# Performance work log

Hardware: AMD Instinct MI355X
Metric: run time of the kernel (lower is better)

The kernel has to match this reference:

```python
import jax, jax.numpy as jnp
import numpy as np

FP8_MAX = 448.0  # max finite value of float8_e4m3fn
EPS = 1e-12


def _quantize_fp8(t):
    """Per-tensor dynamic fp8 quantization: returns (fp8_tensor, scale) where
    dequant = fp8.astype(f32) / scale, matching the torch module's math."""
    t32 = t.astype(jnp.float32)
    amax = jnp.maximum(jnp.max(jnp.abs(t32)), EPS)
    scale = FP8_MAX / amax
    t_fp8 = jnp.clip(t32 * scale, -FP8_MAX, FP8_MAX).astype(jnp.float8_e4m3fn)
    return t_fp8, scale


def setup_inputs() -> dict:
    key = jax.random.key(0)
    kx, kw, kb = jax.random.split(key, 3)
    M, K, N = 4096, 4096, 4096  # tokens, in_features, out_features
    x = jax.random.normal(kx, (M, K), dtype=jnp.float16)
    weight = jax.random.normal(kw, (N, K), dtype=jnp.float16)
    bias = jax.random.normal(kb, (N,), dtype=jnp.float16)
    return {"x": x, "weight": weight, "bias": bias}


def reference(x, weight, bias):
    # weight pre-quantization (quantize_weight)
    w_fp8, w_scale = _quantize_fp8(weight)
    # dynamic activation quantization
    x_fp8, x_scale = _quantize_fp8(x)
    # scaled_mm: (x_fp8 @ w_fp8.T) * scale_a * scale_b, out fp16
    acc = jnp.einsum(
        "mk,nk->mn",
        x_fp8.astype(jnp.float32),
        w_fp8.astype(jnp.float32),
        preferred_element_type=jnp.float32,
    )
    out = (acc * (1.0 / x_scale) * (1.0 / w_scale)).astype(jnp.float16)
    out = out + bias
    return out
```

## Files before the change

kernel.cpp:

```cpp
#include <hip/hip_runtime.h>
#include <hip/hip_fp16.h>

typedef __bf16 bf16x8 __attribute__((ext_vector_type(8)));
typedef float f32x4 __attribute__((ext_vector_type(4)));
typedef int i32x8 __attribute__((ext_vector_type(8)));
typedef unsigned short ushort8 __attribute__((ext_vector_type(8)));

#define BM 256
#define BN 128
#define BK 128
#define FP8MAX 448.0f
#define SCALE_ONE 0x7F7F7F7FU
#define A_BYTES (BM * BK)
#define B_BYTES (BN * BK)
#define SLOT_BYTES (A_BYTES + B_BYTES)

__global__ __launch_bounds__(256)
void amax_stage1(const float* __restrict__ x, unsigned n4x,
                 const float* __restrict__ w, unsigned n4w,
                 float* __restrict__ bm) {
    __shared__ float wmax[4];
    bool isw = blockIdx.x >= 1024;
    const float* in = isw ? w : x;
    unsigned n4 = isw ? n4w : n4x;
    unsigned tid = (blockIdx.x & 1023) * 256 + threadIdx.x;
    float m = 0.f;
    for (unsigned i = tid; i < n4; i += 1024 * 256) {
        float4 v = *(const float4*)(in + (size_t)i * 4);
        m = fmaxf(m, fmaxf(fmaxf(fabsf(v.x), fabsf(v.y)), fmaxf(fabsf(v.z), fabsf(v.w))));
    }
#pragma unroll
    for (int off = 32; off > 0; off >>= 1)
        m = fmaxf(m, __shfl_down(m, off));
    if ((threadIdx.x & 63) == 0) wmax[threadIdx.x >> 6] = m;
    __syncthreads();
    if (threadIdx.x == 0)
        bm[blockIdx.x] = fmaxf(fmaxf(wmax[0], wmax[1]), fmaxf(wmax[2], wmax[3]));
}

__global__ __launch_bounds__(256)
void amax_stage2(const float* __restrict__ bm, float* __restrict__ outv) {
    __shared__ float wmax[4];
    const float* p = bm + (size_t)blockIdx.x * 1024;
    float m = 0.f;
    for (int i = threadIdx.x; i < 1024; i += 256) m = fmaxf(m, p[i]);
#pragma unroll
    for (int off = 32; off > 0; off >>= 1)
        m = fmaxf(m, __shfl_down(m, off));
    if ((threadIdx.x & 63) == 0) wmax[threadIdx.x >> 6] = m;
    __syncthreads();
    if (threadIdx.x == 0)
        outv[blockIdx.x] = fmaxf(fmaxf(wmax[0], wmax[1]), fmaxf(wmax[2], wmax[3]));
}

__global__ __launch_bounds__(256)
void quant_kernel(const float* __restrict__ x, unsigned n8x,
                  const float* __restrict__ w, unsigned n8w,
                  unsigned char* __restrict__ xq, unsigned char* __restrict__ wq,
                  const float* __restrict__ amax2) {
    bool isw = blockIdx.x >= 2048;
    const float* in = isw ? w : x;
    uint2* out = (uint2*)(isw ? wq : xq);
    unsigned n8 = isw ? n8w : n8x;
    float amax = fmaxf(amax2[isw ? 1 : 0], 1e-12f);
    float scale = FP8MAX / amax;
    unsigned tid = (blockIdx.x & 2047) * 256 + threadIdx.x;
    for (unsigned i = tid; i < n8; i += 2048 * 256) {
        float4 lo = *(const float4*)(in + (size_t)i * 8);
        float4 hi = *(const float4*)(in + (size_t)i * 8 + 4);
        float f[8] = {lo.x, lo.y, lo.z, lo.w, hi.x, hi.y, hi.z, hi.w};
#pragma unroll
        for (int j = 0; j < 8; ++j)
            f[j] = fminf(fmaxf(f[j] * scale, -FP8MAX), FP8MAX);
        unsigned w0 = __builtin_amdgcn_cvt_pk_fp8_f32(f[0], f[1], 0u, false);
        w0 = __builtin_amdgcn_cvt_pk_fp8_f32(f[2], f[3], w0, true);
        unsigned w1 = __builtin_amdgcn_cvt_pk_fp8_f32(f[4], f[5], 0u, false);
        w1 = __builtin_amdgcn_cvt_pk_fp8_f32(f[6], f[7], w1, true);
        out[i] = make_uint2(w0, w1);
    }
}

__device__ inline void gl2lds16(const void* g, void* l) {
    __builtin_amdgcn_global_load_lds(
        (const __attribute__((address_space(1))) unsigned int*)g,
        (__attribute__((address_space(3))) unsigned int*)l, 16, 0, 0);
}

__global__ __launch_bounds__(512, 2)
void gemm_kernel(const unsigned char* __restrict__ A,
                 const unsigned char* __restrict__ B,
                 const float* __restrict__ bias,
                 float* __restrict__ C,
                 const float* __restrict__ amax2,
                 int M, int N, int K) {
    extern __shared__ char LDS[];

    int tid = threadIdx.x;
    int lane = tid & 63;
    int wave = tid >> 6;
    int wr = wave >> 1;
    int wc = wave & 1;
    int row0 = blockIdx.y * BM;
    int col0 = blockIdx.x * BN;

    f32x4 acc[4][4];
#pragma unroll
    for (int m = 0; m < 4; ++m)
#pragma unroll
        for (int n = 0; n < 4; ++n)
            acc[m][n] = (f32x4){0.f, 0.f, 0.f, 0.f};

    int frow = lane & 15;
    int g32 = (lane >> 4) * 32;

    const int NT = K >> 7;

    auto STAGE = [&](int t, int si) {
        char* slot = LDS + si * SLOT_BYTES;
#pragma unroll
        for (int i = 0; i < 4; ++i) {
            int s = i * 512 + tid;
            int r = s >> 3, c = s & 7;
            gl2lds16(A + (size_t)(row0 + r) * K + t * BK + ((c ^ (r & 7)) << 4),
                     slot + s * 16);
        }
#pragma unroll
        for (int i = 0; i < 2; ++i) {
            int s = i * 512 + tid;
            int r = s >> 3, c = s & 7;
            gl2lds16(B + (size_t)(col0 + r) * K + t * BK + ((c ^ (r & 7)) << 4),
                     slot + A_BYTES + s * 16);
        }
    };

    STAGE(0, 0);
    if (NT > 1) {
        STAGE(1, 1);
        __builtin_amdgcn_sched_barrier(0);
        asm volatile("s_waitcnt vmcnt(6)" ::: "memory");
    } else {
        __builtin_amdgcn_sched_barrier(0);
        asm volatile("s_waitcnt vmcnt(0)" ::: "memory");
    }
    __builtin_amdgcn_s_barrier();
    __builtin_amdgcn_sched_barrier(0);

    int cur = 0;
    for (int t = 0; t < NT; ++t) {
        if (t + 2 < NT) {
            int stg = (cur == 0) ? 2 : cur - 1;
            STAGE(t + 2, stg);
        }

        char* As = LDS + cur * SLOT_BYTES;
        char* Bs = As + A_BYTES;
        union U { i32x8 v; uint4 q[2]; };
        U af[4], bf[4];
#pragma unroll
        for (int m = 0; m < 4; ++m) {
            int row = wr * 64 + m * 16 + frow;
            int c0 = g32 ^ ((row & 7) << 4);
            const char* p = As + row * 128;
            af[m].q[0] = *(const uint4*)(p + c0);
            af[m].q[1] = *(const uint4*)(p + (c0 ^ 16));
        }
#pragma unroll
        for (int n = 0; n < 4; ++n) {
            int row = wc * 64 + n * 16 + frow;
            int c0 = g32 ^ ((row & 7) << 4);
            const char* p = Bs + row * 128;
            bf[n].q[0] = *(const uint4*)(p + c0);
            bf[n].q[1] = *(const uint4*)(p + (c0 ^ 16));
        }

        __builtin_amdgcn_s_setprio(1);
#pragma unroll
        for (int m = 0; m < 4; ++m)
#pragma unroll
            for (int n = 0; n < 4; ++n)
                acc[m][n] = __builtin_amdgcn_mfma_scale_f32_16x16x128_f8f6f4(
                    af[m].v, bf[n].v, acc[m][n],
                    0, 0, 0, SCALE_ONE, 0, SCALE_ONE);
        __builtin_amdgcn_s_setprio(0);

        if (t + 1 < NT) {
            __builtin_amdgcn_sched_barrier(0);
            if (t + 2 < NT)
                asm volatile("s_waitcnt vmcnt(6)" ::: "memory");
            else
                asm volatile("s_waitcnt vmcnt(0)" ::: "memory");
            __builtin_amdgcn_s_barrier();
            __builtin_amdgcn_sched_barrier(0);
        }
        cur = (cur == 2) ? 0 : cur + 1;
    }

    float ax = fmaxf(amax2[0], 1e-12f);
    float aw = fmaxf(amax2[1], 1e-12f);
    float rs = (ax / FP8MAX) * (aw / FP8MAX);

    int crow0 = row0 + wr * 64;
    int ccol0 = col0 + wc * 64 + frow;
    int rsub = (lane >> 4) * 4;
#pragma unroll
    for (int n = 0; n < 4; ++n) {
        int col = ccol0 + n * 16;
        float bv = bias[col];
#pragma unroll
        for (int m = 0; m < 4; ++m) {
#pragma unroll
            for (int j = 0; j < 4; ++j) {
                int row = crow0 + m * 16 + rsub + j;
                float tcl = __half2float(__float2half_rn(acc[m][n][j] * rs));
                C[(size_t)row * N + col] = __half2float(__float2half_rn(tcl + bv));
            }
        }
    }
}

__device__ inline ushort8 quant8f_bf16(float4 lo, float4 hi, float scale) {
    float f[8] = {lo.x, lo.y, lo.z, lo.w, hi.x, hi.y, hi.z, hi.w};
    ushort8 r;
#pragma unroll
    for (int j = 0; j < 4; ++j) {
        float f0 = fminf(fmaxf(f[2 * j] * scale, -FP8MAX), FP8MAX);
        float f1 = fminf(fmaxf(f[2 * j + 1] * scale, -FP8MAX), FP8MAX);
        unsigned pk = __builtin_amdgcn_cvt_pk_fp8_f32(f0, f1, 0u, false);
        float d0 = __builtin_amdgcn_cvt_f32_fp8(pk, 0);
        float d1 = __builtin_amdgcn_cvt_f32_fp8(pk, 1);
        r[2 * j]     = (unsigned short)(__float_as_uint(d0) >> 16);
        r[2 * j + 1] = (unsigned short)(__float_as_uint(d1) >> 16);
    }
    return r;
}

__global__ __launch_bounds__(256)
void gemm_fused(const float* __restrict__ X, const float* __restrict__ W,
                const float* __restrict__ bias, float* __restrict__ C,
                const float* __restrict__ amax2, int M, int N, int K) {
    __shared__ ushort8 As8[128 * 64 / 8];
    __shared__ ushort8 Bs8[128 * 64 / 8];
    char* As = (char*)As8;
    char* Bs = (char*)Bs8;

    float ax = fmaxf(amax2[0], 1e-12f);
    float aw = fmaxf(amax2[1], 1e-12f);
    float sx = FP8MAX / ax, sw = FP8MAX / aw;

    int tid = threadIdx.x;
    int lane = tid & 63;
    int wave = tid >> 6;
    int row0 = blockIdx.y * 128;
    int col0 = blockIdx.x * 128;
    int wr = wave >> 1, wc = wave & 1;

    f32x4 acc[4][4];
#pragma unroll
    for (int m = 0; m < 4; ++m)
#pragma unroll
        for (int n = 0; n < 4; ++n)
            acc[m][n] = (f32x4){0.f, 0.f, 0.f, 0.f};

    int frow = lane & 15;
    int fksub = (lane >> 4) * 16;

    for (int kt = 0; kt < K; kt += 64) {
#pragma unroll
        for (int i = 0; i < 4; ++i) {
            int s = i * 256 + tid;
            int r = s >> 3, c = s & 7;
            const float* pa = X + (size_t)(row0 + r) * K + kt + c * 8;
            const float* pb = W + (size_t)(col0 + r) * K + kt + c * 8;
            float4 a0 = *(const float4*)pa, a1 = *(const float4*)(pa + 4);
            float4 b0 = *(const float4*)pb, b1 = *(const float4*)(pb + 4);
            *(ushort8*)(As + s * 16) = quant8f_bf16(a0, a1, sx);
            *(ushort8*)(Bs + s * 16) = quant8f_bf16(b0, b1, sw);
        }
        __syncthreads();

#pragma unroll
        for (int kk = 0; kk < 2; ++kk) {
            bf16x8 af[4], bfr[4];
#pragma unroll
            for (int m = 0; m < 4; ++m)
                af[m] = *(const bf16x8*)(As + (wr * 64 + m * 16 + frow) * 128 + kk * 64 + fksub);
#pragma unroll
            for (int n = 0; n < 4; ++n)
                bfr[n] = *(const bf16x8*)(Bs + (wc * 64 + n * 16 + frow) * 128 + kk * 64 + fksub);
#pragma unroll
            for (int m = 0; m < 4; ++m)
#pragma unroll
                for (int n = 0; n < 4; ++n)
                    acc[m][n] = __builtin_amdgcn_mfma_f32_16x16x32_bf16(af[m], bfr[n], acc[m][n], 0, 0, 0);
        }
        __syncthreads();
    }

    float rs = (ax / FP8MAX) * (aw / FP8MAX);
    int crow0 = row0 + wr * 64;
    int ccol0 = col0 + wc * 64 + frow;
    int rsub = (lane >> 4) * 4;
#pragma unroll
    for (int n = 0; n < 4; ++n) {
        int col = ccol0 + n * 16;
        float bv = bias[col];
#pragma unroll
        for (int m = 0; m < 4; ++m) {
#pragma unroll
            for (int j = 0; j < 4; ++j) {
                int row = crow0 + m * 16 + rsub + j;
                float t = __half2float(__float2half_rn(acc[m][n][j] * rs));
                C[(size_t)row * N + col] = __half2float(__float2half_rn(t + bv));
            }
        }
    }
}

extern "C" void kernel_launch(void* const* d_in, const int* in_sizes, int n_in,
                              void* d_out, int out_size, void* d_ws, size_t ws_size,
                              hipStream_t stream) {
    const float* x = (const float*)d_in[0];
    const float* w = (const float*)d_in[1];
    const float* bias = (const float*)d_in[2];
    float* out = (float*)d_out;

    int N = in_sizes[2];
    int K = in_sizes[1] / N;
    int M = in_sizes[0] / K;

    float* bm = (float*)d_ws;
    float* amax2 = bm + 2048;
    unsigned char* xq = (unsigned char*)d_ws + 16384;
    unsigned char* wq = xq + (size_t)M * K;

    unsigned n4x = (unsigned)((size_t)M * K / 4);
    unsigned n4w = (unsigned)((size_t)N * K / 4);

    amax_stage1<<<2048, 256, 0, stream>>>(x, n4x, w, n4w, bm);
    amax_stage2<<<2, 256, 0, stream>>>(bm, amax2);

    size_t needA = (size_t)M * K + (size_t)N * K + 16384;

    if (ws_size >= needA && (M % BM) == 0 && (N % BN) == 0 && (K % BK) == 0 && K / BK >= 2) {
        quant_kernel<<<4096, 256, 0, stream>>>(x, (unsigned)((size_t)M * K / 8),
                                               w, (unsigned)((size_t)N * K / 8),
                                               xq, wq, amax2);
        dim3 grid(N / BN, M / BM);
        gemm_kernel<<<grid, 512, 3 * SLOT_BYTES, stream>>>(xq, wq, bias, out, amax2, M, N, K);
    } else {
        dim3 grid(N / 128, M / 128);
        gemm_fused<<<grid, 256, 0, stream>>>(x, w, bias, out, amax2, M, N, K);
    }
}
```

Before: 145.4 us.

## Enlarge GEMM tile to 256x256 with XCD-aware block swizzle and double buffering

Grows the output tile from 256x128 to 256x256, with each wave now covering 128 rows by 64 columns (8x4 MFMA tiles), which raises arithmetic intensity per LDS load. The grid becomes a 1D launch with an XCD-aware swizzle so that neighbouring tiles land on the same XCD for L2 reuse. The pipeline drops from triple buffering with hand-placed vmcnt waits to double buffering with __syncthreads, and A-fragment loads are software-pipelined two steps ahead inside the MFMA loop. In exchange, the larger accumulator raises register pressure and may cut occupancy, and the simpler sync gives less overlap between loads and compute. There are only 256 workgroups, which may leave some CUs idle on a 256-CU part.

After: 130.3 us. 1.12x faster.

```diff
diff --git a/kernel.cpp b/kernel.cpp
--- a/kernel.cpp
+++ b/kernel.cpp
@@ -7,7 +7,7 @@
 typedef unsigned short ushort8 __attribute__((ext_vector_type(8)));
 
 #define BM 256
-#define BN 128
+#define BN 256
 #define BK 128
 #define FP8MAX 448.0f
 #define SCALE_ONE 0x7F7F7F7FU
@@ -98,14 +98,20 @@
     int tid = threadIdx.x;
     int lane = tid & 63;
     int wave = tid >> 6;
-    int wr = wave >> 1;
-    int wc = wave & 1;
-    int row0 = blockIdx.y * BM;
-    int col0 = blockIdx.x * BN;
-
-    f32x4 acc[4][4];
-#pragma unroll
-    for (int m = 0; m < 4; ++m)
+    int wr = wave >> 2;
+    int wcl = wave & 3;
+
+    int nwg = gridDim.x;
+    int nbx = N / BN;
+    int q = nwg >> 3, r = nwg & 7;
+    int xcd = blockIdx.x & 7, pos = blockIdx.x >> 3;
+    int swz = (xcd < r ? xcd * (q + 1) : r * (q + 1) + (xcd - r) * q) + pos;
+    int row0 = (swz / nbx) * BM;
+    int col0 = (swz % nbx) * BN;
+
+    f32x4 acc[8][4];
+#pragma unroll
+    for (int m = 0; m < 8; ++m)
 #pragma unroll
         for (int n = 0; n < 4; ++n)
             acc[m][n] = (f32x4){0.f, 0.f, 0.f, 0.f};
@@ -120,94 +126,76 @@
 #pragma unroll
         for (int i = 0; i < 4; ++i) {
             int s = i * 512 + tid;
-            int r = s >> 3, c = s & 7;
-            gl2lds16(A + (size_t)(row0 + r) * K + t * BK + ((c ^ (r & 7)) << 4),
+            int rr = s >> 3, c = s & 7;
+            gl2lds16(A + (size_t)(row0 + rr) * K + t * BK + ((c ^ (rr & 7)) << 4),
                      slot + s * 16);
         }
 #pragma unroll
-        for (int i = 0; i < 2; ++i) {
+        for (int i = 0; i < 4; ++i) {
             int s = i * 512 + tid;
-            int r = s >> 3, c = s & 7;
-            gl2lds16(B + (size_t)(col0 + r) * K + t * BK + ((c ^ (r & 7)) << 4),
+            int rr = s >> 3, c = s & 7;
+            gl2lds16(B + (size_t)(col0 + rr) * K + t * BK + ((c ^ (rr & 7)) << 4),
                      slot + A_BYTES + s * 16);
         }
     };
 
+    union U { i32x8 v; uint4 q[2]; };
+    auto LDF = [&](U& u, const char* base, int row) {
+        int c0 = g32 ^ ((row & 7) << 4);
+        const char* p = base + row * 128;
+        u.q[0] = *(const uint4*)(p + c0);
+        u.q[1] = *(const uint4*)(p + (c0 ^ 16));
+    };
+
     STAGE(0, 0);
-    if (NT > 1) {
-        STAGE(1, 1);
-        __builtin_amdgcn_sched_barrier(0);
-        asm volatile("s_waitcnt vmcnt(6)" ::: "memory");
-    } else {
-        __builtin_amdgcn_sched_barrier(0);
-        asm volatile("s_waitcnt vmcnt(0)" ::: "memory");
-    }
-    __builtin_amdgcn_s_barrier();
-    __builtin_amdgcn_sched_barrier(0);
+    __syncthreads();
 
     int cur = 0;
     for (int t = 0; t < NT; ++t) {
-        if (t + 2 < NT) {
-            int stg = (cur == 0) ? 2 : cur - 1;
-            STAGE(t + 2, stg);
-        }
-
-        char* As = LDS + cur * SLOT_BYTES;
-        char* Bs = As + A_BYTES;
-        union U { i32x8 v; uint4 q[2]; };
-        U af[4], bf[4];
-#pragma unroll
-        for (int m = 0; m < 4; ++m) {
-            int row = wr * 64 + m * 16 + frow;
-            int c0 = g32 ^ ((row & 7) << 4);
-            const char* p = As + row * 128;
-            af[m].q[0] = *(const uint4*)(p + c0);
-            af[m].q[1] = *(const uint4*)(p + (c0 ^ 16));
-        }
-#pragma unroll
-        for (int n = 0; n < 4; ++n) {
-            int row = wc * 64 + n * 16 + frow;
-            int c0 = g32 ^ ((row & 7) << 4);
-            const char* p = Bs + row * 128;
-            bf[n].q[0] = *(const uint4*)(p + c0);
-            bf[n].q[1] = *(const uint4*)(p + (c0 ^ 16));
-        }
+        if (t + 1 < NT) STAGE(t + 1, cur ^ 1);
+
+        const char* As = LDS + cur * SLOT_BYTES;
+        const char* Bs = As + A_BYTES;
+
+        U bf[4];
+#pragma unroll
+        for (int n = 0; n < 4; ++n)
+            LDF(bf[n], Bs, wcl * 64 + n * 16 + frow);
+
+        U af[8];
+        LDF(af[0], As, wr * 128 + frow);
+        LDF(af[1], As, wr * 128 + 16 + frow);
 
         __builtin_amdgcn_s_setprio(1);
 #pragma unroll
-        for (int m = 0; m < 4; ++m)
+        for (int m = 0; m < 8; ++m) {
+            if (m + 2 < 8)
+                LDF(af[m + 2], As, wr * 128 + (m + 2) * 16 + frow);
 #pragma unroll
             for (int n = 0; n < 4; ++n)
                 acc[m][n] = __builtin_amdgcn_mfma_scale_f32_16x16x128_f8f6f4(
                     af[m].v, bf[n].v, acc[m][n],
                     0, 0, 0, SCALE_ONE, 0, SCALE_ONE);
+        }
         __builtin_amdgcn_s_setprio(0);
 
-        if (t + 1 < NT) {
-            __builtin_amdgcn_sched_barrier(0);
-            if (t + 2 < NT)
-                asm volatile("s_waitcnt vmcnt(6)" ::: "memory");
-            else
-                asm volatile("s_waitcnt vmcnt(0)" ::: "memory");
-            __builtin_amdgcn_s_barrier();
-            __builtin_amdgcn_sched_barrier(0);
-        }
-        cur = (cur == 2) ? 0 : cur + 1;
+        __syncthreads();
+        cur ^= 1;
     }
 
     float ax = fmaxf(amax2[0], 1e-12f);
     float aw = fmaxf(amax2[1], 1e-12f);
     float rs = (ax / FP8MAX) * (aw / FP8MAX);
 
-    int crow0 = row0 + wr * 64;
-    int ccol0 = col0 + wc * 64 + frow;
+    int crow0 = row0 + wr * 128;
+    int ccol0 = col0 + wcl * 64 + frow;
     int rsub = (lane >> 4) * 4;
 #pragma unroll
     for (int n = 0; n < 4; ++n) {
         int col = ccol0 + n * 16;
         float bv = bias[col];
 #pragma unroll
-        for (int m = 0; m < 4; ++m) {
+        for (int m = 0; m < 8; ++m) {
 #pragma unroll
             for (int j = 0; j < 4; ++j) {
                 int row = crow0 + m * 16 + rsub + j;
@@ -345,8 +333,8 @@
         quant_kernel<<<4096, 256, 0, stream>>>(x, (unsigned)((size_t)M * K / 8),
                                                w, (unsigned)((size_t)N * K / 8),
                                                xq, wq, amax2);
-        dim3 grid(N / BN, M / BM);
-        gemm_kernel<<<grid, 512, 3 * SLOT_BYTES, stream>>>(xq, wq, bias, out, amax2, M, N, K);
+        int nwg = (M / BM) * (N / BN);
+        gemm_kernel<<<nwg, 512, 2 * SLOT_BYTES, stream>>>(xq, wq, bias, out, amax2, M, N, K);
     } else {
         dim3 grid(N / 128, M / 128);
         gemm_fused<<<grid, 256, 0, stream>>>(x, w, bias, out, amax2, M, N, K);
```
